# Performance work log

Measured on AMD Instinct MI355X. Metric: run time of the kernel, lower is better.

## Reference

```python
import jax, jax.numpy as jnp
import numpy as np

N_USERS = 100000
N_ITEMS = 50000
D = 128          # n_factors
L = 200          # hist_len
B = 2048
SIGMA = 0.1      # hyper_approx (posterior lognormal scale)
PRIOR = 1.0      # hyper_prior (prior lognormal scale)
TAU = 4.0
EPS = 1e-8
LN_EPS = 1e-5


def _layernorm(x, gamma, beta):
    m = jnp.mean(x, axis=-1, keepdims=True)
    v = jnp.var(x, axis=-1, keepdims=True)
    return (x - m) * jax.lax.rsqrt(v + LN_EPS) * gamma + beta


def setup_inputs() -> dict:
    key = jax.random.key(0)
    ks = jax.random.split(key, 20)
    user_idx = jax.random.randint(ks[0], (B,), 0, N_USERS, dtype=jnp.int32)
    item_idx = jax.random.randint(ks[1], (B,), 0, N_ITEMS, dtype=jnp.int32)
    # user_hist buffer: per-user ragged history padded with N_ITEMS
    lengths = jax.random.randint(ks[2], (N_USERS,), 1, L + 1, dtype=jnp.int32)
    raw_hist = jax.random.randint(ks[3], (N_USERS, L), 0, N_ITEMS, dtype=jnp.int32)
    pos = jnp.arange(L, dtype=jnp.int32)
    user_hist = jnp.where(pos[None, :] < lengths[:, None], raw_hist, N_ITEMS).astype(jnp.int32)
    # embeddings (padding rows zeroed, std=0.01 init)
    user_embed = 0.01 * jax.random.normal(ks[4], (N_USERS + 1, D), dtype=jnp.float32)
    user_embed = user_embed.at[N_USERS].set(0.0)
    item_embed = 0.01 * jax.random.normal(ks[5], (N_ITEMS + 1, D), dtype=jnp.float32)
    item_embed = item_embed.at[N_ITEMS].set(0.0)
    s = 1.0 / np.sqrt(D)
    W_i = s * jax.random.normal(ks[6], (D, D), dtype=jnp.float32)
    W_h = s * jax.random.normal(ks[7], (D, D), dtype=jnp.float32)
    # BAM 'concat' (additive) score params: v^T tanh(Wq q + Wk k)
    Wq = s * jax.random.normal(ks[8], (D, D), dtype=jnp.float32)
    Wk = s * jax.random.normal(ks[9], (D, D), dtype=jnp.float32)
    v_attn = s * jax.random.normal(ks[10], (D,), dtype=jnp.float32)
    pred_W = s * jax.random.normal(ks[11], (D,), dtype=jnp.float32)
    pred_b = jnp.zeros((), dtype=jnp.float32)
    gamma_u = jnp.ones((D,), jnp.float32); beta_u = jnp.zeros((D,), jnp.float32)
    gamma_i = jnp.ones((D,), jnp.float32); beta_i = jnp.zeros((D,), jnp.float32)
    # reparameterization noise (forward uses stochastic=True)
    noise_u = jax.random.normal(ks[12], (B, L), dtype=jnp.float32)
    noise_i = jax.random.normal(ks[13], (B, L), dtype=jnp.float32)
    return dict(user_idx=user_idx, item_idx=item_idx, user_hist=user_hist,
                user_embed=user_embed, item_embed=item_embed, W_i=W_i, W_h=W_h,
                Wq=Wq, Wk=Wk, v_attn=v_attn, pred_W=pred_W, pred_b=pred_b,
                gamma_u=gamma_u, beta_u=beta_u, gamma_i=gamma_i, beta_i=beta_i,
                noise_u=noise_u, noise_i=noise_i)


def reference(user_idx, item_idx, user_hist, user_embed, item_embed, W_i, W_h,
              Wq, Wk, v_attn, pred_W, pred_b, gamma_u, beta_u, gamma_i, beta_i,
              noise_u, noise_i):
    maskf_dummy = None  # (placeholder, no-op)
    hist = user_hist[user_idx]                                   # (B, L) int
    mask = (hist != item_idx[:, None]) & (hist != N_ITEMS)       # (B, L) bool
    maskf = mask.astype(jnp.float32)

    u_id = user_embed[user_idx]                                  # (B, D)
    t_raw = item_embed[item_idx]                                 # (B, D)
    h_raw = item_embed[hist]                                     # (B, L, D)
    t_id = t_raw @ W_i.T                                         # W_i(target)
    h_id = h_raw @ W_h.T                                         # W_h(hist)

    def bam(q, K, V, noise):
        # additive ('concat') scoring: v . tanh(q Wq + K Wk), temperature tau
        h = jnp.tanh((q @ Wq.T)[:, None, :] + jnp.einsum('bld,ed->ble', K, Wk))
        scores = jnp.einsum('ble,e->bl', h, v_attn) / TAU        # (B, L)
        scores = jnp.where(mask, scores, -1e9)
        phi = jax.nn.softmax(scores, axis=-1)                    # (B, L)
        mu = jnp.log(phi + EPS)
        w = jnp.exp(mu + SIGMA * noise) * maskf                  # lognormal sample
        attn = w / (jnp.sum(w, axis=-1, keepdims=True) + EPS)
        out = jnp.einsum('bl,bld->bd', attn, V)                  # (B, D)
        # KL( LN(mu, SIGMA) || LN(0, PRIOR) ) over valid positions
        kl_el = jnp.log(PRIOR / SIGMA) + (SIGMA ** 2 + mu ** 2) / (2.0 * PRIOR ** 2) - 0.5
        kl = jnp.sum(kl_el * maskf) / (jnp.sum(maskf) + EPS)
        return out, kl

    u_hist, kl_u = bam(u_id, h_id, h_id, noise_u)
    i_hist, kl_i = bam(t_id, h_id, h_id, noise_i)
    u = _layernorm(u_hist * u_id, gamma_u, beta_u)
    i = _layernorm(i_hist * t_id, gamma_i, beta_i)
    logit = (u * i) @ pred_W + pred_b                            # (B,)
    return logit, 0.5 * (kl_u + kl_i)
```

## Files before the change

### kernel.cpp

```cpp
#include <hip/hip_runtime.h>

#define B_ 2048
#define L_ 200
#define D_ 128
#define NITEMS 50000

typedef __attribute__((ext_vector_type(8))) short short8v;
typedef __attribute__((ext_vector_type(4))) float floatx4;
typedef __attribute__((ext_vector_type(4))) int intx4;

__device__ __forceinline__ short f2bf(float f) {
    union { float f; unsigned u; } v;
    v.f = f;
    unsigned r = v.u + 0x7FFFu + ((v.u >> 16) & 1u);
    return (short)(r >> 16);
}
__device__ __forceinline__ float bf2f(unsigned short s) {
    union { unsigned u; float f; } v;
    v.u = ((unsigned)s) << 16;
    return v.f;
}

__device__ __forceinline__ float tanh5(float x) {
    const float x2 = x * x;
    const float p = __builtin_fmaf(x2, 0.13333333f, -0.33333333f);
    return __builtin_fmaf(x * x2, p, x);
}

__device__ __forceinline__ float wave_sum(float v) {
#pragma unroll
    for (int m = 32; m >= 1; m >>= 1) v += __shfl_xor(v, m, 64);
    return v;
}

__device__ __forceinline__ void gload_lds16(const short* g, short* l) {
    __builtin_amdgcn_global_load_lds(
        (const __attribute__((address_space(1))) void*)g,
        (__attribute__((address_space(3))) void*)l, 16, 0, 0);
}

__device__ __forceinline__ intx4 ds_read16(const short* p) {
    intx4 d;
    asm volatile("ds_read_b128 %0, %1"
                 : "=v"(d)
                 : "v"((const __attribute__((address_space(3))) short*)p));
    return d;
}

__global__ __launch_bounds__(256) void k01(const float* __restrict__ Wk,
                                           const float* __restrict__ Wh,
                                           short* __restrict__ Mbf,
                                           const float* __restrict__ src,
                                           short* __restrict__ dst, int n8) {
    const int t = threadIdx.x;
    if (blockIdx.x < 128) {
        __shared__ float wk[128];
        const int e = blockIdx.x;
        if (t < 128) wk[t] = Wk[e * 128 + t];
        __syncthreads();
        if (t < 128) {
            float s = 0.f;
#pragma unroll 4
            for (int d = 0; d < 128; ++d) s += wk[d] * Wh[d * 128 + t];
            Mbf[e * 128 + t] = f2bf(s);
        }
        return;
    }
    const int i = (blockIdx.x - 128) * 256 + t;
    if (i >= n8) return;
    const float4 f0 = *reinterpret_cast<const float4*>(src + i * 8);
    const float4 f1 = *reinterpret_cast<const float4*>(src + i * 8 + 4);
    short8v w;
    w[0] = f2bf(f0.x); w[1] = f2bf(f0.y); w[2] = f2bf(f0.z); w[3] = f2bf(f0.w);
    w[4] = f2bf(f1.x); w[5] = f2bf(f1.y); w[6] = f2bf(f1.z); w[7] = f2bf(f1.w);
    *reinterpret_cast<short8v*>(dst + i * 8) = w;
}

__global__ __launch_bounds__(256) void k2_prep(
    const int* __restrict__ user_idx, const int* __restrict__ item_idx,
    const int* __restrict__ user_hist, const float* __restrict__ user_embed,
    const float* __restrict__ item_embed, const float* __restrict__ W_i,
    const float* __restrict__ Wq, float* __restrict__ uid_o,
    float* __restrict__ tid_o, float* __restrict__ qu_o, float* __restrict__ qt_o,
    int* __restrict__ hist_o) {
    const int bb = blockIdx.x * 4, t = threadIdx.x;
    __shared__ float uid_s[4][128], traw_s[4][128], tid_s[4][128];
    __shared__ int uis[4], iis[4];
    if (t < 4) {
        uis[t] = user_idx[bb + t];
        iis[t] = item_idx[bb + t];
    }
    __syncthreads();
#pragma unroll
    for (int c = 0; c < 2; ++c) {
        const int idx = c * 256 + t;
        const int bs = idx >> 7, e = idx & 127;
        const float uv = user_embed[(long)uis[bs] * 128 + e];
        uid_s[bs][e] = uv;
        traw_s[bs][e] = item_embed[(long)iis[bs] * 128 + e];
        uid_o[(bb + bs) * 128 + e] = uv;
    }
    for (int l0 = t; l0 < 800; l0 += 256) {
        const int bs = (l0 >= 200) + (l0 >= 400) + (l0 >= 600);
        hist_o[bb * 200 + l0] = user_hist[(long)uis[bs] * 200 + (l0 - bs * 200)];
    }
    __syncthreads();
    {
        const int half = t >> 7, e = t & 127;
        const float* Wrow = (half ? Wq : W_i) + e * 128;
        float acc[4] = {0.f, 0.f, 0.f, 0.f};
        for (int c = 0; c < 128; c += 4) {
            const float4 w = *reinterpret_cast<const float4*>(Wrow + c);
#pragma unroll
            for (int k = 0; k < 4; ++k) {
                const float4 s = half ? *reinterpret_cast<const float4*>(&uid_s[k][c])
                                      : *reinterpret_cast<const float4*>(&traw_s[k][c]);
                acc[k] += w.x * s.x + w.y * s.y + w.z * s.z + w.w * s.w;
            }
        }
#pragma unroll
        for (int k = 0; k < 4; ++k) {
            if (half) qu_o[(bb + k) * 128 + e] = acc[k];
            else {
                tid_s[k][e] = acc[k];
                tid_o[(bb + k) * 128 + e] = acc[k];
            }
        }
    }
    __syncthreads();
    {
        const int half = t >> 7, e = t & 127;
        const float* Wrow = Wq + e * 128;
        float acc[2] = {0.f, 0.f};
        for (int c = 0; c < 128; c += 4) {
            const float4 w = *reinterpret_cast<const float4*>(Wrow + c);
#pragma unroll
            for (int k = 0; k < 2; ++k) {
                const float4 s = *reinterpret_cast<const float4*>(&tid_s[half * 2 + k][c]);
                acc[k] += w.x * s.x + w.y * s.y + w.z * s.z + w.w * s.w;
            }
        }
#pragma unroll
        for (int k = 0; k < 2; ++k) qt_o[(bb + half * 2 + k) * 128 + e] = acc[k];
    }
}

__global__ __launch_bounds__(512) void k345(
    const short* __restrict__ Mbf, const short* __restrict__ item_bf,
    const int* __restrict__ hist_g, const int* __restrict__ item_idx,
    const float* __restrict__ qu_, const float* __restrict__ qt_,
    const float* __restrict__ v_attn, const float* __restrict__ noise_u,
    const float* __restrict__ noise_i, const float* __restrict__ W_h,
    const float* __restrict__ uid, const float* __restrict__ tid,
    const float* __restrict__ gamma_u, const float* __restrict__ beta_u,
    const float* __restrict__ gamma_i, const float* __restrict__ beta_i,
    const float* __restrict__ pred_W, const float* __restrict__ pred_b,
    float* __restrict__ klu, float* __restrict__ kli, float* __restrict__ msm,
    float* __restrict__ out) {
    __shared__ __align__(16) short M_lds[8][4][4][16][8];
    __shared__ __align__(16) char scratch[32768];
    __shared__ float q_lds[2][2][128];
    __shared__ float v_lds[128];
    __shared__ int hgs[400];
    __shared__ float scL[2 * 400];
    __shared__ float attL[2 * 400];
    __shared__ float red[8];

    const int t = threadIdx.x, blk = blockIdx.x;
    const int b0 = blk * 2;
    const int ii0 = item_idx[b0], ii1 = item_idx[b0 + 1];

#pragma unroll
    for (int c4 = 0; c4 < 4; ++c4) {
        const int flat = c4 * 512 + t;
        const int lo2 = flat & 15, g = (flat >> 4) & 3, ks = (flat >> 6) & 3, t8 = flat >> 8;
        *reinterpret_cast<short8v*>(&M_lds[t8][ks][g][lo2][0]) =
            *reinterpret_cast<const short8v*>(Mbf + (t8 * 16 + lo2) * 128 + ks * 32 + g * 8);
    }
    {
        const int bs = t >> 8, side = (t >> 7) & 1, e = t & 127;
        q_lds[bs][side][e] =
            side ? qt_[(b0 + bs) * 128 + e] : qu_[(b0 + bs) * 128 + e];
    }
    if (t < 128) v_lds[t] = v_attn[t];
    if (t < 400) hgs[t] = hist_g[blk * 400 + t];
    __syncthreads();

    const int wid = t >> 6, lane = t & 63;
    const int lo = lane & 15, hi = lane >> 4;

    {
        const int nt = (wid == 7) ? 4 : 3;
        short* wbase = reinterpret_cast<short*>(scratch) + wid * 2048;
        const char* itemc = (const char*)item_bf;

        int ro[4];
#pragma unroll
        for (int i = 0; i < 4; ++i) {
            const int lt = wid * 3 + ((i < 3) ? i : 3);
            ro[i] = hgs[min(lt, 24) * 16 + lo];
        }
        auto stage = [&](int i) {
            const char* rp = itemc + ((long)ro[i] << 8) + hi * 16;
#pragma unroll
            for (int ks = 0; ks < 4; ++ks)
                gload_lds16((const short*)(rp + ks * 64), wbase + ks * 512);
        };

        stage(0);
        for (int i = 0; i < nt; ++i) {
            asm volatile("s_waitcnt vmcnt(0)" ::: "memory");
            __builtin_amdgcn_sched_barrier(0);
            const short* pb = wbase + hi * 128 + lo * 8;
            intx4 r0 = ds_read16(pb);
            intx4 r1 = ds_read16(pb + 512);
            intx4 r2 = ds_read16(pb + 1024);
            intx4 r3 = ds_read16(pb + 1536);
            asm volatile("s_waitcnt lgkmcnt(0)" ::: "memory");
            __builtin_amdgcn_sched_barrier(0);
            short8v f[4];
            f[0] = __builtin_bit_cast(short8v, r0);
            f[1] = __builtin_bit_cast(short8v, r1);
            f[2] = __builtin_bit_cast(short8v, r2);
            f[3] = __builtin_bit_cast(short8v, r3);
            if (i + 1 < nt) stage(i + 1);
            __builtin_amdgcn_sched_barrier(0);

            const int lr = (wid * 3 + i) * 16 + lo;
            const int bs = lr >= 200;
            float su = 0.f, si = 0.f;
#pragma unroll
            for (int h2 = 0; h2 < 2; ++h2) {
                floatx4 acc[4];
#pragma unroll
                for (int q4 = 0; q4 < 4; ++q4) acc[q4] = (floatx4){0.f, 0.f, 0.f, 0.f};
#pragma unroll
                for (int ks = 0; ks < 4; ++ks)
#pragma unroll
                    for (int q4 = 0; q4 < 4; ++q4)
                        acc[q4] = __builtin_amdgcn_mfma_f32_16x16x32_bf16(
                            *reinterpret_cast<const short8v*>(&M_lds[h2 * 4 + q4][ks][hi][lo][0]),
                            f[ks], acc[q4], 0, 0, 0);
#pragma unroll
                for (int q4 = 0; q4 < 4; ++q4) {
                    const int t8 = h2 * 4 + q4;
                    const floatx4 vv = *reinterpret_cast<const floatx4*>(&v_lds[t8 * 16 + hi * 4]);
                    const floatx4 qa = *reinterpret_cast<const floatx4*>(&q_lds[bs][0][t8 * 16 + hi * 4]);
                    const floatx4 qb = *reinterpret_cast<const floatx4*>(&q_lds[bs][1][t8 * 16 + hi * 4]);
#pragma unroll
                    for (int rg = 0; rg < 4; ++rg) {
                        su = __builtin_fmaf(vv[rg], tanh5(qa[rg] + acc[q4][rg]), su);
                        si = __builtin_fmaf(vv[rg], tanh5(qb[rg] + acc[q4][rg]), si);
                    }
                }
            }
            su += __shfl_xor(su, 16, 64);
            su += __shfl_xor(su, 32, 64);
            si += __shfl_xor(si, 16, 64);
            si += __shfl_xor(si, 32, 64);
            if (hi == 0) {
                scL[lr] = su * 0.25f;
                scL[400 + lr] = si * 0.25f;
            }
        }
    }
    __syncthreads();

    if (wid < 4) {
        const int bs = wid & 1, side = wid >> 1;
        const int bb = b0 + bs;
        const int iiv = bs ? ii1 : ii0;
        const float* nz = (side ? noise_i : noise_u) + bb * L_;
        const float* scl = scL + side * 400 + bs * 200;
        const int* hrow = hgs + bs * 200;

        float mk[4], s2[4];
        float msl = 0.f, esum = 0.f;
#pragma unroll
        for (int k = 0; k < 4; ++k) {
            const int l = lane + 64 * k;
            const int hv = (l < L_) ? hrow[l] : NITEMS;
            mk[k] = (l < L_ && hv != iiv && hv != NITEMS) ? 1.f : 0.f;
            msl += mk[k];
            const float s = (mk[k] > 0.5f) ? scl[(l < L_) ? l : 0] : -1e9f;
            s2[k] = s * 1.4426950f;
            esum += exp2f(s2[k]);
        }
        const float msum = wave_sum(msl);
        float Z = wave_sum(esum);
        Z = fmaxf(Z, 1e-37f);
        const float z2 = log2f(Z);

        float wv[4], wsum = 0.f, klsum = 0.f;
#pragma unroll
        for (int k = 0; k < 4; ++k) {
            const int l = lane + 64 * k;
            const int lm = (l < L_) ? l : 0;
            const float d = s2[k] - z2;
            wv[k] = exp2f(__builtin_fmaf(nz[lm], 0.14426950f, d)) * mk[k];
            wsum += wv[k];
            klsum += (1.8075851f + 0.2402265f * d * d) * mk[k];
        }
        const float Zw = wave_sum(wsum);
        const float kls = wave_sum(klsum);
        const float invZw = 1.f / (Zw + 1e-8f);
#pragma unroll
        for (int k = 0; k < 4; ++k) {
            const int l = lane + 64 * k;
            if (l < L_) attL[side * 400 + bs * 200 + l] = wv[k] * invZw;
        }
        if (lane == 0) {
            if (side == 0) { klu[bb] = kls; msm[bb] = msum; }
            else kli[bb] = kls;
        }
    }
    __syncthreads();

    float* P = reinterpret_cast<float*>(scratch);
    {
        const int bs = wid >> 2, rg = wid & 3, c2 = lane;
        const float* a0p = attL + bs * 200;
        const float* a1p = attL + 400 + bs * 200;
        const int* hrow = hgs + bs * 200;
        float s00 = 0.f, s01 = 0.f, s10 = 0.f, s11 = 0.f;
#pragma unroll
        for (int c = 0; c < 2; ++c) {
            const int lb = rg * 50 + c * 25;
            unsigned hv[25];
#pragma unroll
            for (int j = 0; j < 25; ++j)
                hv[j] = *reinterpret_cast<const unsigned*>(
                    item_bf + (long)hrow[lb + j] * 128 + c2 * 2);
#pragma unroll
            for (int j = 0; j < 25; ++j) {
                const float h0 = __uint_as_float(hv[j] << 16);
                const float h1 = __uint_as_float(hv[j] & 0xffff0000u);
                const float a0 = a0p[lb + j], a1 = a1p[lb + j];
                s00 += a0 * h0; s01 += a0 * h1;
                s10 += a1 * h0; s11 += a1 * h1;
            }
        }
        P[((bs * 2 + 0) * 4 + rg) * 128 + c2 * 2] = s00;
        P[((bs * 2 + 0) * 4 + rg) * 128 + c2 * 2 + 1] = s01;
        P[((bs * 2 + 1) * 4 + rg) * 128 + c2 * 2] = s10;
        P[((bs * 2 + 1) * 4 + rg) * 128 + c2 * 2 + 1] = s11;
    }
    __syncthreads();

    const int bs3 = t >> 8, side3 = (t >> 7) & 1, tl = t & 127;
    const int grp = t >> 7;
    {
        const int gidx = (bs3 * 2 + side3) * 4;
        float a = P[(gidx + 0) * 128 + tl] + P[(gidx + 1) * 128 + tl] +
                  P[(gidx + 2) * 128 + tl] + P[(gidx + 3) * 128 + tl];
        __syncthreads();
        P[2048 + grp * 128 + tl] = a;
    }
    __syncthreads();

    float x;
    {
        const float* vsrc = P + 2048 + grp * 128;
        float o = 0.f;
#pragma unroll 2
        for (int c = 0; c < 128; c += 4) {
            const float4 w = *reinterpret_cast<const float4*>(&W_h[tl * 128 + c]);
            o += w.x * vsrc[c] + w.y * vsrc[c + 1] + w.z * vsrc[c + 2] + w.w * vsrc[c + 3];
        }
        x = o * (side3 ? tid[(b0 + bs3) * 128 + tl] : uid[(b0 + bs3) * 128 + tl]);
    }
    const float v1 = wave_sum(x);
    if (lane == 0) red[wid] = v1;
    __syncthreads();
    const float mean = (red[grp * 2] + red[grp * 2 + 1]) * (1.f / 128.f);
    const float d = x - mean;
    const float v2 = wave_sum(d * d);
    __syncthreads();
    if (lane == 0) red[wid] = v2;
    __syncthreads();
    const float var = (red[grp * 2] + red[grp * 2 + 1]) * (1.f / 128.f);
    const float gmm = side3 ? gamma_i[tl] : gamma_u[tl];
    const float bta = side3 ? beta_i[tl] : beta_u[tl];
    const float uin = d * rsqrtf(var + 1e-5f) * gmm + bta;
    __syncthreads();
    P[2560 + grp * 128 + tl] = uin;
    __syncthreads();
    float p = 0.f;
    if (t < 256) {
        const int bs = t >> 7, tl2 = t & 127;
        p = P[2560 + (bs * 2 + 0) * 128 + tl2] * P[2560 + (bs * 2 + 1) * 128 + tl2] *
            pred_W[tl2];
    }
    const float v3 = wave_sum(p);
    if (lane == 0 && wid < 4) red[4 + wid] = v3;
    __syncthreads();
    if (t == 0) out[b0] = red[4] + red[5] + pred_b[0];
    if (t == 1) out[b0 + 1] = red[6] + red[7] + pred_b[0];
}

__global__ __launch_bounds__(256) void k6_kl(const float* __restrict__ klu,
                                             const float* __restrict__ kli,
                                             const float* __restrict__ msm,
                                             float* __restrict__ out) {
    __shared__ float red[4];
    const int t = threadIdx.x;
    float su = 0.f, si = 0.f, sm = 0.f;
    for (int b = t; b < B_; b += 256) {
        su += klu[b];
        si += kli[b];
        sm += msm[b];
    }
    su = wave_sum(su);
    si = wave_sum(si);
    sm = wave_sum(sm);
    __syncthreads();
    if ((t & 63) == 0) red[t >> 6] = su;
    __syncthreads();
    su = red[0] + red[1] + red[2] + red[3];
    __syncthreads();
    if ((t & 63) == 0) red[t >> 6] = si;
    __syncthreads();
    si = red[0] + red[1] + red[2] + red[3];
    __syncthreads();
    if ((t & 63) == 0) red[t >> 6] = sm;
    __syncthreads();
    sm = red[0] + red[1] + red[2] + red[3];
    if (t == 0) {
        const float inv = 1.f / (sm + 1e-8f);
        out[0] = 0.5f * (su * inv + si * inv);
    }
}

extern "C" void kernel_launch(void* const* d_in, const int* in_sizes, int n_in,
                              void* d_out, int out_size, void* d_ws, size_t ws_size,
                              hipStream_t stream) {
    const int* user_idx = (const int*)d_in[0];
    const int* item_idx = (const int*)d_in[1];
    const int* user_hist = (const int*)d_in[2];
    const float* user_embed = (const float*)d_in[3];
    const float* item_embed = (const float*)d_in[4];
    const float* W_i = (const float*)d_in[5];
    const float* W_h = (const float*)d_in[6];
    const float* Wq = (const float*)d_in[7];
    const float* Wk = (const float*)d_in[8];
    const float* v_attn = (const float*)d_in[9];
    const float* pred_W = (const float*)d_in[10];
    const float* pred_b = (const float*)d_in[11];
    const float* gamma_u = (const float*)d_in[12];
    const float* beta_u = (const float*)d_in[13];
    const float* gamma_i = (const float*)d_in[14];
    const float* beta_i = (const float*)d_in[15];
    const float* noise_u = (const float*)d_in[16];
    const float* noise_i = (const float*)d_in[17];
    float* out = (float*)d_out;

    char* ws = (char*)d_ws;
    size_t off = 0;
    auto alloc = [&](size_t bytes) -> void* {
        void* p = ws + off;
        off = (off + bytes + 255) & ~(size_t)255;
        return p;
    };
    short* Mbf     = (short*)alloc(128 * 128 * 2);
    short* item_bf = (short*)alloc((size_t)(NITEMS + 1) * 128 * 2);
    float* uid = (float*)alloc((size_t)B_ * 128 * 4);
    float* tid = (float*)alloc((size_t)B_ * 128 * 4);
    float* qu  = (float*)alloc((size_t)B_ * 128 * 4);
    float* qt  = (float*)alloc((size_t)B_ * 128 * 4);
    int* hg    = (int*)alloc((size_t)B_ * L_ * 4);
    float* klu = (float*)alloc((size_t)B_ * 4);
    float* kli = (float*)alloc((size_t)B_ * 4);
    float* msm = (float*)alloc((size_t)B_ * 4);

    const int n8 = (NITEMS + 1) * 128 / 8;
    const int ncvt = (n8 + 255) / 256;
    k01<<<128 + ncvt, 256, 0, stream>>>(Wk, W_h, Mbf, item_embed, item_bf, n8);
    k2_prep<<<B_ / 4, 256, 0, stream>>>(user_idx, item_idx, user_hist, user_embed,
                                        item_embed, W_i, Wq, uid, tid, qu, qt, hg);
    k345<<<B_ / 2, 512, 0, stream>>>(Mbf, item_bf, hg, item_idx, qu, qt, v_attn,
                                     noise_u, noise_i, W_h, uid, tid, gamma_u, beta_u,
                                     gamma_i, beta_i, pred_W, pred_b, klu, kli, msm, out);
    k6_kl<<<1, 256, 0, stream>>>(klu, kli, msm, out + B_);
}
```

Before: 103.1 us.

## Skip score tiles and weighted-sum chunks covering only padded history positions

Marks each 16-row history tile that holds at least one real item (not padding, not the target item) and compacts those tiles into a list. The eight waves then stride over this list with a double-buffered staging loop instead of a fixed three or four tiles each. The attention-weighted sum also skips 25-row chunks that begin past the row's valid history length. Both changes target work spent on padded positions. The cost is an extra shared-memory pass, two barriers, a serial list build on one thread, and uneven load across waves.

Result: slower. 106.7 us (+3.5%).

```diff
diff --git a/kernel.cpp b/kernel.cpp
--- a/kernel.cpp
+++ b/kernel.cpp
@@ -14,11 +14,6 @@
     v.f = f;
     unsigned r = v.u + 0x7FFFu + ((v.u >> 16) & 1u);
     return (short)(r >> 16);
-}
-__device__ __forceinline__ float bf2f(unsigned short s) {
-    union { unsigned u; float f; } v;
-    v.u = ((unsigned)s) << 16;
-    return v.f;
 }
 
 __device__ __forceinline__ float tanh5(float x) {
@@ -165,6 +160,10 @@
     __shared__ float scL[2 * 400];
     __shared__ float attL[2 * 400];
     __shared__ float red[8];
+    __shared__ unsigned char neededB[32];
+    __shared__ int tlist_s[25];
+    __shared__ int nv_s;
+    __shared__ int len_s[2];
 
     const int t = threadIdx.x, blk = blockIdx.x;
     const int b0 = blk * 2;
@@ -184,31 +183,103 @@
     }
     if (t < 128) v_lds[t] = v_attn[t];
     if (t < 400) hgs[t] = hist_g[blk * 400 + t];
+    if (t < 32) neededB[t] = 0;
     __syncthreads();
 
     const int wid = t >> 6, lane = t & 63;
     const int lo = lane & 15, hi = lane >> 4;
 
-    {
-        const int nt = (wid == 7) ? 4 : 3;
+    if (t < 400) {
+        const int iiv = (t >= 200) ? ii1 : ii0;
+        const int hv = hgs[t];
+        if (hv != NITEMS && hv != iiv) neededB[t >> 4] = 1;
+    }
+    if (wid < 2) {
+        const int bs = wid;
+        int cnt = 0;
+#pragma unroll
+        for (int k = 0; k < 4; ++k) {
+            const int l = lane + 64 * k;
+            cnt += (l < 200 && hgs[bs * 200 + l] != NITEMS) ? 1 : 0;
+        }
+        float c = wave_sum((float)cnt);
+        if (lane == 0) len_s[bs] = (int)c;
+    }
+    __syncthreads();
+    if (t == 0) {
+        int n = 0;
+#pragma unroll 1
+        for (int j = 0; j < 25; ++j)
+            if (neededB[j]) tlist_s[n++] = j;
+        nv_s = n;
+    }
+    __syncthreads();
+
+    {
+        const int nv = nv_s;
         short* wbase = reinterpret_cast<short*>(scratch) + wid * 2048;
         const char* itemc = (const char*)item_bf;
 
-        int ro[4];
-#pragma unroll
-        for (int i = 0; i < 4; ++i) {
-            const int lt = wid * 3 + ((i < 3) ? i : 3);
-            ro[i] = hgs[min(lt, 24) * 16 + lo];
-        }
-        auto stage = [&](int i) {
-            const char* rp = itemc + ((long)ro[i] << 8) + hi * 16;
+        auto stageo = [&](int ro) {
+            const char* rp = itemc + ((long)ro << 8) + hi * 16;
 #pragma unroll
             for (int ks = 0; ks < 4; ++ks)
                 gload_lds16((const short*)(rp + ks * 64), wbase + ks * 512);
         };
 
-        stage(0);
-        for (int i = 0; i < nt; ++i) {
+        auto compute_store = [&](int tile, const short8v f[4]) {
+            const int lr = tile * 16 + lo;
+            const int bs = lr >= 200;
+            float su = 0.f, si = 0.f;
+#pragma unroll
+            for (int h2 = 0; h2 < 2; ++h2) {
+                floatx4 acc[4];
+#pragma unroll
+                for (int q4 = 0; q4 < 4; ++q4) acc[q4] = (floatx4){0.f, 0.f, 0.f, 0.f};
+#pragma unroll
+                for (int ks = 0; ks < 4; ++ks)
+#pragma unroll
+                    for (int q4 = 0; q4 < 4; ++q4)
+                        acc[q4] = __builtin_amdgcn_mfma_f32_16x16x32_bf16(
+                            *reinterpret_cast<const short8v*>(&M_lds[h2 * 4 + q4][ks][hi][lo][0]),
+                            f[ks], acc[q4], 0, 0, 0);
+#pragma unroll
+                for (int q4 = 0; q4 < 4; ++q4) {
+                    const int t8 = h2 * 4 + q4;
+                    const floatx4 vv = *reinterpret_cast<const floatx4*>(&v_lds[t8 * 16 + hi * 4]);
+                    const floatx4 qa = *reinterpret_cast<const floatx4*>(&q_lds[bs][0][t8 * 16 + hi * 4]);
+                    const floatx4 qb = *reinterpret_cast<const floatx4*>(&q_lds[bs][1][t8 * 16 + hi * 4]);
+#pragma unroll
+                    for (int rg = 0; rg < 4; ++rg) {
+                        su = __builtin_fmaf(vv[rg], tanh5(qa[rg] + acc[q4][rg]), su);
+                        si = __builtin_fmaf(vv[rg], tanh5(qb[rg] + acc[q4][rg]), si);
+                    }
+                }
+            }
+            su += __shfl_xor(su, 16, 64);
+            su += __shfl_xor(su, 32, 64);
+            si += __shfl_xor(si, 16, 64);
+            si += __shfl_xor(si, 32, 64);
+            if (hi == 0) {
+                scL[lr] = su * 0.25f;
+                scL[400 + lr] = si * 0.25f;
+            }
+        };
+
+        int kcur = wid;
+        int tile_cur = 0;
+        if (kcur < nv) {
+            tile_cur = tlist_s[kcur];
+            stageo(hgs[tile_cur * 16 + lo]);
+        }
+        while (kcur < nv) {
+            const int knext = kcur + 8;
+            const bool has_next = knext < nv;
+            int tile_next = 0, ro_next = 0;
+            if (has_next) {
+                tile_next = tlist_s[knext];
+                ro_next = hgs[tile_next * 16 + lo];
+            }
             asm volatile("s_waitcnt vmcnt(0)" ::: "memory");
             __builtin_amdgcn_sched_barrier(0);
             const short* pb = wbase + hi * 128 + lo * 8;
@@ -223,45 +294,11 @@
             f[1] = __builtin_bit_cast(short8v, r1);
             f[2] = __builtin_bit_cast(short8v, r2);
             f[3] = __builtin_bit_cast(short8v, r3);
-            if (i + 1 < nt) stage(i + 1);
+            if (has_next) stageo(ro_next);
             __builtin_amdgcn_sched_barrier(0);
-
-            const int lr = (wid * 3 + i) * 16 + lo;
-            const int bs = lr >= 200;
-            float su = 0.f, si = 0.f;
-#pragma unroll
-            for (int h2 = 0; h2 < 2; ++h2) {
-                floatx4 acc[4];
-#pragma unroll
-                for (int q4 = 0; q4 < 4; ++q4) acc[q4] = (floatx4){0.f, 0.f, 0.f, 0.f};
-#pragma unroll
-                for (int ks = 0; ks < 4; ++ks)
-#pragma unroll
-                    for (int q4 = 0; q4 < 4; ++q4)
-                        acc[q4] = __builtin_amdgcn_mfma_f32_16x16x32_bf16(
-                            *reinterpret_cast<const short8v*>(&M_lds[h2 * 4 + q4][ks][hi][lo][0]),
-                            f[ks], acc[q4], 0, 0, 0);
-#pragma unroll
-                for (int q4 = 0; q4 < 4; ++q4) {
-                    const int t8 = h2 * 4 + q4;
-                    const floatx4 vv = *reinterpret_cast<const floatx4*>(&v_lds[t8 * 16 + hi * 4]);
-                    const floatx4 qa = *reinterpret_cast<const floatx4*>(&q_lds[bs][0][t8 * 16 + hi * 4]);
-                    const floatx4 qb = *reinterpret_cast<const floatx4*>(&q_lds[bs][1][t8 * 16 + hi * 4]);
-#pragma unroll
-                    for (int rg = 0; rg < 4; ++rg) {
-                        su = __builtin_fmaf(vv[rg], tanh5(qa[rg] + acc[q4][rg]), su);
-                        si = __builtin_fmaf(vv[rg], tanh5(qb[rg] + acc[q4][rg]), si);
-                    }
-                }
-            }
-            su += __shfl_xor(su, 16, 64);
-            su += __shfl_xor(su, 32, 64);
-            si += __shfl_xor(si, 16, 64);
-            si += __shfl_xor(si, 32, 64);
-            if (hi == 0) {
-                scL[lr] = su * 0.25f;
-                scL[400 + lr] = si * 0.25f;
-            }
+            compute_store(tile_cur, f);
+            kcur = knext;
+            tile_cur = tile_next;
         }
     }
     __syncthreads();
@@ -322,22 +359,25 @@
         const float* a0p = attL + bs * 200;
         const float* a1p = attL + 400 + bs * 200;
         const int* hrow = hgs + bs * 200;
+        const int lenb = len_s[bs];
         float s00 = 0.f, s01 = 0.f, s10 = 0.f, s11 = 0.f;
 #pragma unroll
         for (int c = 0; c < 2; ++c) {
             const int lb = rg * 50 + c * 25;
-            unsigned hv[25];
-#pragma unroll
-            for (int j = 0; j < 25; ++j)
-                hv[j] = *reinterpret_cast<const unsigned*>(
-                    item_bf + (long)hrow[lb + j] * 128 + c2 * 2);
-#pragma unroll
-            for (int j = 0; j < 25; ++j) {
-                const float h0 = __uint_as_float(hv[j] << 16);
-                const float h1 = __uint_as_float(hv[j] & 0xffff0000u);
-                const float a0 = a0p[lb + j], a1 = a1p[lb + j];
-                s00 += a0 * h0; s01 += a0 * h1;
-                s10 += a1 * h0; s11 += a1 * h1;
+            if (lb < lenb) {
+                unsigned hv[25];
+#pragma unroll
+                for (int j = 0; j < 25; ++j)
+                    hv[j] = *reinterpret_cast<const unsigned*>(
+                        item_bf + (long)hrow[lb + j] * 128 + c2 * 2);
+#pragma unroll
+                for (int j = 0; j < 25; ++j) {
+                    const float h0 = __uint_as_float(hv[j] << 16);
+                    const float h1 = __uint_as_float(hv[j] & 0xffff0000u);
+                    const float a0 = a0p[lb + j], a1 = a1p[lb + j];
+                    s00 += a0 * h0; s01 += a0 * h1;
+                    s10 += a1 * h0; s11 += a1 * h1;
+                }
             }
         }
         P[((bs * 2 + 0) * 4 + rg) * 128 + c2 * 2] = s00;
```
